# Kernel optimization log

Measured on AMD Instinct MI355X. Metric: run time of the kernel, lower is better.

The kernel has to match this reference:

```python
import jax, jax.numpy as jnp
import numpy as np

NUM_CLUSTERS = 64
DIM = 512
ALPHA = 100.0
EPS = 1e-12  # torch F.normalize eps


def setup_inputs() -> dict:
    key = jax.random.key(0)
    k1, k2 = jax.random.split(key)
    x1 = jax.random.normal(k1, (30, DIM, 28, 28), dtype=jnp.float32)
    centroids = jax.random.uniform(k2, (NUM_CLUSTERS, DIM), dtype=jnp.float32)
    # _init_params: conv weight = 2*alpha*centroids (1x1 conv), bias = -alpha*||centroid||
    conv_w = 2.0 * ALPHA * centroids
    conv_b = -ALPHA * jnp.linalg.norm(centroids, axis=1)
    return {"x1": x1, "centroids": centroids, "conv_w": conv_w, "conv_b": conv_b}


def _l2norm(v, axis):
    n = jnp.sqrt(jnp.sum(v * v, axis=axis, keepdims=True))
    return v / jnp.maximum(n, EPS)


def reference(x1, centroids, conv_w, conv_b):
    T, C, H, W = x1.shape
    K, D = centroids.shape
    x = x1.reshape(T, C, H * W)            # [T, C, N]
    x = _l2norm(x, axis=1)                 # normalize_input: L2 over channel dim
    # 1x1 conv == matmul over channels: logits [T, K, N]
    logits = jnp.einsum('kc,tcn->tkn', conv_w, x) + conv_b[None, :, None]
    a = jax.nn.softmax(logits, axis=1)     # soft assignment over clusters
    # vlad[t,k,c] = sum_n a[t,k,n]*(x[t,c,n] - centroids[k,c])
    # rewritten as two small matmuls, avoiding the [K,C,N] residual tensor
    vlad = jnp.einsum('tkn,tcn->tkc', a, x) - a.sum(axis=-1)[:, :, None] * centroids[None]
    vlad = _l2norm(vlad, axis=2)           # intra-normalization over feature dim
    v = vlad.reshape(T, K * D)
    v = _l2norm(v, axis=1)                 # global L2 normalization
    return v.sum(axis=0, keepdims=True)    # [1, K*D] accumulated over 30 timesteps
```

## Files before the change

kernel.cpp:

```cpp
#include <hip/hip_runtime.h>
#include <math.h>

#define T_ 30
#define C_ 512
#define N_ 784
#define NA_ 800
#define SPITCH 72
#define EPSV 1e-12f

typedef __attribute__((ext_vector_type(8))) short bf16x8;
typedef __attribute__((ext_vector_type(4))) float f32x4;

__device__ __forceinline__ unsigned short f2bf(float f) {
    union { float f; unsigned int u; } v; v.f = f;
    unsigned int r = (v.u + 0x7FFFu + ((v.u >> 16) & 1u)) >> 16;
    return (unsigned short)r;
}
__device__ __forceinline__ float bf2f(unsigned short h) {
    union { unsigned int u; float f; } v; v.u = ((unsigned int)h) << 16;
    return v.f;
}

__global__ void k_prep(const float* __restrict__ w, unsigned short* __restrict__ wh,
                       unsigned short* __restrict__ wl) {
    int idx = blockIdx.x * 256 + threadIdx.x;
    float v = w[idx];
    unsigned short h = f2bf(v);
    wh[idx] = h;
    wl[idx] = f2bf(v - bf2f(h));
}

__global__ __launch_bounds__(256, 4) void k_assign(
    const float* __restrict__ x, const unsigned short* __restrict__ wh,
    const unsigned short* __restrict__ wl, const float* __restrict__ b,
    unsigned short* __restrict__ aT, float* __restrict__ asum)
{
    __shared__ __align__(16) char smem[2 * 4 * 16 * SPITCH * 2];
    unsigned short* xh = (unsigned short*)smem;
    unsigned short* xl = xh + 4 * 16 * SPITCH;
    float* red = (float*)smem;
    __shared__ float ssq[4][16];

    int t = blockIdx.y, n0 = blockIdx.x * 16;
    int tid = threadIdx.x;
    int w = tid >> 6, L = tid & 63, lid = L & 15, quad = L >> 4;
    int cbase = w * 128;
    int nseg = (L & 3) * 4;
    int crow = L >> 2;

    const float* xb = x + (size_t)t * C_ * N_ + n0 + nseg;
    unsigned short* shh = xh + w * 16 * SPITCH;
    unsigned short* shl = xl + w * 16 * SPITCH;
    const unsigned short* wha = wh + (size_t)lid * C_ + cbase + quad * 8;
    const unsigned short* wla = wl + (size_t)lid * C_ + cbase + quad * 8;

    float bk = b[L];
    float ss0 = 0.f, ss1 = 0.f, ss2 = 0.f, ss3 = 0.f;
    f32x4 acc[4];
    #pragma unroll
    for (int mt = 0; mt < 4; ++mt)
        #pragma unroll
        for (int r = 0; r < 4; ++r) acc[mt][r] = 0.f;

    #pragma unroll
    for (int half = 0; half < 2; ++half) {
        float4 q[4];
        #pragma unroll
        for (int p = 0; p < 4; ++p)
            q[p] = *reinterpret_cast<const float4*>(
                xb + (size_t)(cbase + half * 64 + p * 16 + crow) * N_);
        #pragma unroll
        for (int p = 0; p < 4; ++p) {
            int cl = p * 16 + crow;
            float vv[4] = {q[p].x, q[p].y, q[p].z, q[p].w};
            ss0 = fmaf(vv[0], vv[0], ss0); ss1 = fmaf(vv[1], vv[1], ss1);
            ss2 = fmaf(vv[2], vv[2], ss2); ss3 = fmaf(vv[3], vv[3], ss3);
            #pragma unroll
            for (int j = 0; j < 4; ++j) {
                unsigned short h = f2bf(vv[j]);
                shh[(nseg + j) * SPITCH + cl] = h;
                shl[(nseg + j) * SPITCH + cl] = f2bf(vv[j] - bf2f(h));
            }
        }
        #pragma unroll
        for (int ks2 = 0; ks2 < 2; ++ks2) {
            bf16x8 bh = *reinterpret_cast<const bf16x8*>(
                &shh[lid * SPITCH + ks2 * 32 + quad * 8]);
            bf16x8 bl = *reinterpret_cast<const bf16x8*>(
                &shl[lid * SPITCH + ks2 * 32 + quad * 8]);
            int cg = half * 64 + ks2 * 32;
            #pragma unroll
            for (int mt = 0; mt < 4; ++mt) {
                bf16x8 ah = *reinterpret_cast<const bf16x8*>(
                    wha + (size_t)mt * 16 * C_ + cg);
                bf16x8 al = *reinterpret_cast<const bf16x8*>(
                    wla + (size_t)mt * 16 * C_ + cg);
                acc[mt] = __builtin_amdgcn_mfma_f32_16x16x32_bf16(ah, bh, acc[mt], 0, 0, 0);
                acc[mt] = __builtin_amdgcn_mfma_f32_16x16x32_bf16(al, bh, acc[mt], 0, 0, 0);
                acc[mt] = __builtin_amdgcn_mfma_f32_16x16x32_bf16(ah, bl, acc[mt], 0, 0, 0);
            }
        }
    }
    #pragma unroll
    for (int m = 4; m <= 32; m <<= 1) {
        ss0 += __shfl_xor(ss0, m, 64); ss1 += __shfl_xor(ss1, m, 64);
        ss2 += __shfl_xor(ss2, m, 64); ss3 += __shfl_xor(ss3, m, 64);
    }
    if (L < 4) {
        ssq[w][L * 4 + 0] = ss0; ssq[w][L * 4 + 1] = ss1;
        ssq[w][L * 4 + 2] = ss2; ssq[w][L * 4 + 3] = ss3;
    }
    __syncthreads();
    {
        float* rp = red + w * (16 * 68);
        #pragma unroll
        for (int mt = 0; mt < 4; ++mt)
            *reinterpret_cast<f32x4*>(&rp[lid * 68 + mt * 16 + quad * 4]) = acc[mt];
    }
    __syncthreads();

    float vv[4], iv[4];
    #pragma unroll
    for (int i = 0; i < 4; ++i) {
        int n = w * 4 + i;
        float s = ssq[0][n] + ssq[1][n] + ssq[2][n] + ssq[3][n];
        iv[i] = 1.0f / fmaxf(sqrtf(s), EPSV);
        float v = red[0 * 1088 + n * 68 + L] + red[1 * 1088 + n * 68 + L]
                + red[2 * 1088 + n * 68 + L] + red[3 * 1088 + n * 68 + L];
        vv[i] = fmaf(v, iv[i], bk);
    }
    float mx[4] = {vv[0], vv[1], vv[2], vv[3]};
    #pragma unroll
    for (int m = 1; m <= 32; m <<= 1) {
        #pragma unroll
        for (int i = 0; i < 4; ++i) mx[i] = fmaxf(mx[i], __shfl_xor(mx[i], m, 64));
    }
    float e[4], se[4];
    #pragma unroll
    for (int i = 0; i < 4; ++i) { e[i] = __expf(vv[i] - mx[i]); se[i] = e[i]; }
    #pragma unroll
    for (int m = 1; m <= 32; m <<= 1) {
        #pragma unroll
        for (int i = 0; i < 4; ++i) se[i] += __shfl_xor(se[i], m, 64);
    }
    float asl = 0.f;
    unsigned short av[4];
    #pragma unroll
    for (int i = 0; i < 4; ++i) {
        float a = e[i] / se[i];
        av[i] = f2bf(a * iv[i]);
        asl += a;
    }
    atomicAdd(&asum[t * 64 + L], asl);
    ushort4 st; st.x = av[0]; st.y = av[1]; st.z = av[2]; st.w = av[3];
    *reinterpret_cast<ushort4*>(aT + ((size_t)t * 64 + L) * NA_ + n0 + w * 4) = st;
    if (blockIdx.x == 48) {
        ushort4 z; z.x = 0; z.y = 0; z.z = 0; z.w = 0;
        *reinterpret_cast<ushort4*>(aT + ((size_t)t * 64 + L) * NA_ + 784 + w * 4) = z;
    }
}

__global__ __launch_bounds__(256, 4) void k_vlad(
    const float* __restrict__ x, const unsigned short* __restrict__ aT,
    const float* __restrict__ asum, const float* __restrict__ cent,
    float* __restrict__ vlad)
{
    __shared__ float red[4][16 * 68];
    int t = blockIdx.z, nh = blockIdx.y, c0 = blockIdx.x * 16;
    int tid = threadIdx.x;
    int w = tid >> 6, L = tid & 63, lid = L & 15, quad = L >> 4;

    f32x4 acc[4];
    #pragma unroll
    for (int mt = 0; mt < 4; ++mt)
        #pragma unroll
        for (int r = 0; r < 4; ++r) acc[mt][r] = 0.f;

    const float* xrow = x + ((size_t)t * C_ + c0 + lid) * N_;
    const unsigned short* a0 = aT + (size_t)t * 64 * NA_ + (size_t)lid * NA_;

    int k = tid >> 2, cs4 = (tid & 3) * 4;
    float as = nh ? 0.f : asum[t * 64 + k];
    float4 cv = *reinterpret_cast<const float4*>(cent + k * C_ + c0 + cs4);

    int send = nh ? 25 : 13;
    int s0 = nh * 13 + w;

    int nb = s0 * 32 + quad * 8;
    int nc = nb > 776 ? 776 : nb;
    float4 x0c = *reinterpret_cast<const float4*>(xrow + nc);
    float4 x1c = *reinterpret_cast<const float4*>(xrow + nc + 4);
    bf16x8 f0 = *reinterpret_cast<const bf16x8*>(a0 + nb);
    bf16x8 f1 = *reinterpret_cast<const bf16x8*>(a0 + 16 * NA_ + nb);
    bf16x8 f2 = *reinterpret_cast<const bf16x8*>(a0 + 32 * NA_ + nb);
    bf16x8 f3 = *reinterpret_cast<const bf16x8*>(a0 + 48 * NA_ + nb);

    for (int s = s0; s < send; s += 4) {
        int sn = s + 4;
        float4 x0n = x0c, x1n = x1c;
        bf16x8 g0 = f0, g1 = f1, g2v = f2, g3 = f3;
        if (sn < send) {
            int nb2 = sn * 32 + quad * 8;
            int nc2 = nb2 > 776 ? 776 : nb2;
            x0n = *reinterpret_cast<const float4*>(xrow + nc2);
            x1n = *reinterpret_cast<const float4*>(xrow + nc2 + 4);
            g0 = *reinterpret_cast<const bf16x8*>(a0 + nb2);
            g1 = *reinterpret_cast<const bf16x8*>(a0 + 16 * NA_ + nb2);
            g2v = *reinterpret_cast<const bf16x8*>(a0 + 32 * NA_ + nb2);
            g3 = *reinterpret_cast<const bf16x8*>(a0 + 48 * NA_ + nb2);
        }
        bf16x8 bb;
        bb[0] = (short)f2bf(x0c.x); bb[1] = (short)f2bf(x0c.y);
        bb[2] = (short)f2bf(x0c.z); bb[3] = (short)f2bf(x0c.w);
        bb[4] = (short)f2bf(x1c.x); bb[5] = (short)f2bf(x1c.y);
        bb[6] = (short)f2bf(x1c.z); bb[7] = (short)f2bf(x1c.w);
        acc[0] = __builtin_amdgcn_mfma_f32_16x16x32_bf16(f0, bb, acc[0], 0, 0, 0);
        acc[1] = __builtin_amdgcn_mfma_f32_16x16x32_bf16(f1, bb, acc[1], 0, 0, 0);
        acc[2] = __builtin_amdgcn_mfma_f32_16x16x32_bf16(f2, bb, acc[2], 0, 0, 0);
        acc[3] = __builtin_amdgcn_mfma_f32_16x16x32_bf16(f3, bb, acc[3], 0, 0, 0);
        x0c = x0n; x1c = x1n; f0 = g0; f1 = g1; f2 = g2v; f3 = g3;
    }
    {
        float* rp = &red[w][0];
        #pragma unroll
        for (int mt = 0; mt < 4; ++mt)
            *reinterpret_cast<f32x4*>(&rp[lid * 68 + mt * 16 + quad * 4]) = acc[mt];
    }
    __syncthreads();

    float* dst = vlad + ((size_t)t * 64 + k) * C_ + c0 + cs4;
    #pragma unroll
    for (int j = 0; j < 4; ++j) {
        int cc = cs4 + j;
        float v = red[0][cc * 68 + k] + red[1][cc * 68 + k]
                + red[2][cc * 68 + k] + red[3][cc * 68 + k];
        v -= as * ((const float*)&cv)[j];
        atomicAdd(dst + j, v);
    }
}

__global__ __launch_bounds__(256) void k_g2(const float* __restrict__ vlad,
                                            float* __restrict__ g2) {
    int tid = threadIdx.x;
    int w = tid >> 6, L = tid & 63;
    int r = blockIdx.x * 4 + w;
    const float* p = vlad + (size_t)r * C_;
    float s = 0.f;
    #pragma unroll
    for (int i = 0; i < 2; ++i) {
        float4 a = *reinterpret_cast<const float4*>(p + i * 256 + L * 4);
        s = fmaf(a.x, a.x, fmaf(a.y, a.y, fmaf(a.z, a.z, fmaf(a.w, a.w, s))));
    }
    #pragma unroll
    for (int m = 1; m <= 32; m <<= 1) s += __shfl_xor(s, m, 64);
    if (L == 0) g2[r] = s;
}

__global__ __launch_bounds__(256) void k_out(
    const float* __restrict__ vlad, const float* __restrict__ g2,
    float* __restrict__ out)
{
    __shared__ float intr[1920];
    __shared__ float gl[1920];
    __shared__ float sinv[T_];
    __shared__ float part[256];
    int tid = threadIdx.x;
    for (int i = tid; i < 1920; i += 256) {
        float s = g2[i];
        gl[i] = s;
        intr[i] = 1.0f / fmaxf(sqrtf(s), EPSV);
    }
    __syncthreads();
    if (tid < T_) {
        float s = 0.f;
        #pragma unroll 8
        for (int k = 0; k < 64; ++k) {
            float iv = intr[tid * 64 + k];
            s += gl[tid * 64 + k] * iv * iv;
        }
        sinv[tid] = 1.0f / fmaxf(sqrtf(s), EPSV);
    }
    __syncthreads();
    int idx = blockIdx.x * 128 + (tid & 127);
    int th = tid >> 7;
    int k = idx >> 9;
    float s = 0.f;
    #pragma unroll
    for (int t = th * 15; t < th * 15 + 15; ++t)
        s += vlad[(size_t)t * 32768 + idx] * intr[t * 64 + k] * sinv[t];
    part[tid] = s;
    __syncthreads();
    if (tid < 128) out[idx] = part[tid] + part[tid + 128];
}

extern "C" void kernel_launch(void* const* d_in, const int* in_sizes, int n_in,
                              void* d_out, int out_size, void* d_ws, size_t ws_size,
                              hipStream_t stream) {
    const float* x    = (const float*)d_in[0];
    const float* cent = (const float*)d_in[1];
    const float* w    = (const float*)d_in[2];
    const float* b    = (const float*)d_in[3];
    float* out = (float*)d_out;

    char* p = (char*)d_ws;
    unsigned short* wh = (unsigned short*)p;  p += 65536;
    unsigned short* wl = (unsigned short*)p;  p += 65536;
    float* asum = (float*)p;                  p += 1920 * 4;
    float* vlad = (float*)p;                  p += (size_t)T_ * 64 * C_ * 4;
    float* g2   = (float*)p;                  p += 1920 * 4;
    unsigned short* aT = (unsigned short*)p;  p += (size_t)T_ * 64 * NA_ * 2;

    k_prep<<<128, 256, 0, stream>>>(w, wh, wl);
    hipMemsetAsync(asum, 0, 1920 * 4 + (size_t)T_ * 64 * C_ * 4, stream);
    k_assign<<<dim3(49, T_), 256, 0, stream>>>(x, wh, wl, b, aT, asum);
    k_vlad<<<dim3(32, 2, T_), 256, 0, stream>>>(x, aT, asum, cent, vlad);
    k_g2<<<480, 256, 0, stream>>>(vlad, g2);
    k_out<<<256, 256, 0, stream>>>(vlad, g2, out);
}
```

Before: 158.1 us.

## Emit bf16 copy of x in assign kernel and split vlad partials without atomics

```diff
diff --git a/kernel.cpp b/kernel.cpp
--- a/kernel.cpp
+++ b/kernel.cpp
@@ -5,6 +5,7 @@
 #define C_ 512
 #define N_ 784
 #define NA_ 800
+#define XBP 800
 #define SPITCH 72
 #define EPSV 1e-12f
 
@@ -33,7 +34,8 @@
 __global__ __launch_bounds__(256, 4) void k_assign(
     const float* __restrict__ x, const unsigned short* __restrict__ wh,
     const unsigned short* __restrict__ wl, const float* __restrict__ b,
-    unsigned short* __restrict__ aT, float* __restrict__ asum)
+    unsigned short* __restrict__ aT, float* __restrict__ asum,
+    unsigned short* __restrict__ xbh)
 {
     __shared__ __align__(16) char smem[2 * 4 * 16 * SPITCH * 2];
     unsigned short* xh = (unsigned short*)smem;
@@ -49,11 +51,18 @@
     int crow = L >> 2;
 
     const float* xb = x + (size_t)t * C_ * N_ + n0 + nseg;
+    unsigned short* xbrow = xbh + (size_t)t * C_ * XBP + n0 + nseg;
     unsigned short* shh = xh + w * 16 * SPITCH;
     unsigned short* shl = xl + w * 16 * SPITCH;
     const unsigned short* wha = wh + (size_t)lid * C_ + cbase + quad * 8;
     const unsigned short* wla = wl + (size_t)lid * C_ + cbase + quad * 8;
 
+    float4 q[8];
+    #pragma unroll
+    for (int p = 0; p < 8; ++p)
+        q[p] = *reinterpret_cast<const float4*>(
+            xb + (size_t)(cbase + p * 16 + crow) * N_);
+
     float bk = b[L];
     float ss0 = 0.f, ss1 = 0.f, ss2 = 0.f, ss3 = 0.f;
     f32x4 acc[4];
@@ -64,23 +73,24 @@
 
     #pragma unroll
     for (int half = 0; half < 2; ++half) {
-        float4 q[4];
-        #pragma unroll
-        for (int p = 0; p < 4; ++p)
-            q[p] = *reinterpret_cast<const float4*>(
-                xb + (size_t)(cbase + half * 64 + p * 16 + crow) * N_);
         #pragma unroll
         for (int p = 0; p < 4; ++p) {
+            int pp = half * 4 + p;
             int cl = p * 16 + crow;
-            float vv[4] = {q[p].x, q[p].y, q[p].z, q[p].w};
+            int c  = cbase + pp * 16 + crow;
+            float vv[4] = {q[pp].x, q[pp].y, q[pp].z, q[pp].w};
             ss0 = fmaf(vv[0], vv[0], ss0); ss1 = fmaf(vv[1], vv[1], ss1);
             ss2 = fmaf(vv[2], vv[2], ss2); ss3 = fmaf(vv[3], vv[3], ss3);
+            unsigned short hs[4];
             #pragma unroll
             for (int j = 0; j < 4; ++j) {
                 unsigned short h = f2bf(vv[j]);
+                hs[j] = h;
                 shh[(nseg + j) * SPITCH + cl] = h;
                 shl[(nseg + j) * SPITCH + cl] = f2bf(vv[j] - bf2f(h));
             }
+            ushort4 hv; hv.x = hs[0]; hv.y = hs[1]; hv.z = hs[2]; hv.w = hs[3];
+            *reinterpret_cast<ushort4*>(xbrow + (size_t)c * XBP) = hv;
         }
         #pragma unroll
         for (int ks2 = 0; ks2 < 2; ++ks2) {
@@ -157,13 +167,19 @@
     if (blockIdx.x == 48) {
         ushort4 z; z.x = 0; z.y = 0; z.z = 0; z.w = 0;
         *reinterpret_cast<ushort4*>(aT + ((size_t)t * 64 + L) * NA_ + 784 + w * 4) = z;
+        #pragma unroll
+        for (int pp = 0; pp < 8; ++pp) {
+            int c = cbase + pp * 16 + crow;
+            *reinterpret_cast<ushort4*>(
+                xbh + ((size_t)t * C_ + c) * XBP + 784 + nseg) = z;
+        }
     }
 }
 
 __global__ __launch_bounds__(256, 4) void k_vlad(
-    const float* __restrict__ x, const unsigned short* __restrict__ aT,
+    const unsigned short* __restrict__ xbh, const unsigned short* __restrict__ aT,
     const float* __restrict__ asum, const float* __restrict__ cent,
-    float* __restrict__ vlad)
+    float* __restrict__ vlad0, float* __restrict__ vlad1)
 {
     __shared__ float red[4][16 * 68];
     int t = blockIdx.z, nh = blockIdx.y, c0 = blockIdx.x * 16;
@@ -176,7 +192,7 @@
         #pragma unroll
         for (int r = 0; r < 4; ++r) acc[mt][r] = 0.f;
 
-    const float* xrow = x + ((size_t)t * C_ + c0 + lid) * N_;
+    const unsigned short* xrow = xbh + ((size_t)t * C_ + c0 + lid) * XBP;
     const unsigned short* a0 = aT + (size_t)t * 64 * NA_ + (size_t)lid * NA_;
 
     int k = tid >> 2, cs4 = (tid & 3) * 4;
@@ -187,9 +203,7 @@
     int s0 = nh * 13 + w;
 
     int nb = s0 * 32 + quad * 8;
-    int nc = nb > 776 ? 776 : nb;
-    float4 x0c = *reinterpret_cast<const float4*>(xrow + nc);
-    float4 x1c = *reinterpret_cast<const float4*>(xrow + nc + 4);
+    bf16x8 xc = *reinterpret_cast<const bf16x8*>(xrow + nb);
     bf16x8 f0 = *reinterpret_cast<const bf16x8*>(a0 + nb);
     bf16x8 f1 = *reinterpret_cast<const bf16x8*>(a0 + 16 * NA_ + nb);
     bf16x8 f2 = *reinterpret_cast<const bf16x8*>(a0 + 32 * NA_ + nb);
@@ -197,28 +211,21 @@
 
     for (int s = s0; s < send; s += 4) {
         int sn = s + 4;
-        float4 x0n = x0c, x1n = x1c;
+        bf16x8 xn = xc;
         bf16x8 g0 = f0, g1 = f1, g2v = f2, g3 = f3;
         if (sn < send) {
             int nb2 = sn * 32 + quad * 8;
-            int nc2 = nb2 > 776 ? 776 : nb2;
-            x0n = *reinterpret_cast<const float4*>(xrow + nc2);
-            x1n = *reinterpret_cast<const float4*>(xrow + nc2 + 4);
-            g0 = *reinterpret_cast<const bf16x8*>(a0 + nb2);
-            g1 = *reinterpret_cast<const bf16x8*>(a0 + 16 * NA_ + nb2);
+            xn  = *reinterpret_cast<const bf16x8*>(xrow + nb2);
+            g0  = *reinterpret_cast<const bf16x8*>(a0 + nb2);
+            g1  = *reinterpret_cast<const bf16x8*>(a0 + 16 * NA_ + nb2);
             g2v = *reinterpret_cast<const bf16x8*>(a0 + 32 * NA_ + nb2);
-            g3 = *reinterpret_cast<const bf16x8*>(a0 + 48 * NA_ + nb2);
-        }
-        bf16x8 bb;
-        bb[0] = (short)f2bf(x0c.x); bb[1] = (short)f2bf(x0c.y);
-        bb[2] = (short)f2bf(x0c.z); bb[3] = (short)f2bf(x0c.w);
-        bb[4] = (short)f2bf(x1c.x); bb[5] = (short)f2bf(x1c.y);
-        bb[6] = (short)f2bf(x1c.z); bb[7] = (short)f2bf(x1c.w);
-        acc[0] = __builtin_amdgcn_mfma_f32_16x16x32_bf16(f0, bb, acc[0], 0, 0, 0);
-        acc[1] = __builtin_amdgcn_mfma_f32_16x16x32_bf16(f1, bb, acc[1], 0, 0, 0);
-        acc[2] = __builtin_amdgcn_mfma_f32_16x16x32_bf16(f2, bb, acc[2], 0, 0, 0);
-        acc[3] = __builtin_amdgcn_mfma_f32_16x16x32_bf16(f3, bb, acc[3], 0, 0, 0);
-        x0c = x0n; x1c = x1n; f0 = g0; f1 = g1; f2 = g2v; f3 = g3;
+            g3  = *reinterpret_cast<const bf16x8*>(a0 + 48 * NA_ + nb2);
+        }
+        acc[0] = __builtin_amdgcn_mfma_f32_16x16x32_bf16(f0, xc, acc[0], 0, 0, 0);
+        acc[1] = __builtin_amdgcn_mfma_f32_16x16x32_bf16(f1, xc, acc[1], 0, 0, 0);
+        acc[2] = __builtin_amdgcn_mfma_f32_16x16x32_bf16(f2, xc, acc[2], 0, 0, 0);
+        acc[3] = __builtin_amdgcn_mfma_f32_16x16x32_bf16(f3, xc, acc[3], 0, 0, 0);
+        xc = xn; f0 = g0; f1 = g1; f2 = g2v; f3 = g3;
     }
     {
         float* rp = &red[w][0];
@@ -228,28 +235,34 @@
     }
     __syncthreads();
 
-    float* dst = vlad + ((size_t)t * 64 + k) * C_ + c0 + cs4;
+    float* dst = (nh ? vlad1 : vlad0) + ((size_t)t * 64 + k) * C_ + c0 + cs4;
+    float4 vout;
     #pragma unroll
     for (int j = 0; j < 4; ++j) {
         int cc = cs4 + j;
         float v = red[0][cc * 68 + k] + red[1][cc * 68 + k]
                 + red[2][cc * 68 + k] + red[3][cc * 68 + k];
         v -= as * ((const float*)&cv)[j];
-        atomicAdd(dst + j, v);
-    }
-}
-
-__global__ __launch_bounds__(256) void k_g2(const float* __restrict__ vlad,
+        ((float*)&vout)[j] = v;
+    }
+    *reinterpret_cast<float4*>(dst) = vout;
+}
+
+__global__ __launch_bounds__(256) void k_g2(const float* __restrict__ vlad0,
+                                            const float* __restrict__ vlad1,
                                             float* __restrict__ g2) {
     int tid = threadIdx.x;
     int w = tid >> 6, L = tid & 63;
     int r = blockIdx.x * 4 + w;
-    const float* p = vlad + (size_t)r * C_;
+    const float* p0 = vlad0 + (size_t)r * C_;
+    const float* p1 = vlad1 + (size_t)r * C_;
     float s = 0.f;
     #pragma unroll
     for (int i = 0; i < 2; ++i) {
-        float4 a = *reinterpret_cast<const float4*>(p + i * 256 + L * 4);
-        s = fmaf(a.x, a.x, fmaf(a.y, a.y, fmaf(a.z, a.z, fmaf(a.w, a.w, s))));
+        float4 a = *reinterpret_cast<const float4*>(p0 + i * 256 + L * 4);
+        float4 b4 = *reinterpret_cast<const float4*>(p1 + i * 256 + L * 4);
+        float vx = a.x + b4.x, vy = a.y + b4.y, vz = a.z + b4.z, vw = a.w + b4.w;
+        s = fmaf(vx, vx, fmaf(vy, vy, fmaf(vz, vz, fmaf(vw, vw, s))));
     }
     #pragma unroll
     for (int m = 1; m <= 32; m <<= 1) s += __shfl_xor(s, m, 64);
@@ -257,8 +270,8 @@
 }
 
 __global__ __launch_bounds__(256) void k_out(
-    const float* __restrict__ vlad, const float* __restrict__ g2,
-    float* __restrict__ out)
+    const float* __restrict__ vlad0, const float* __restrict__ vlad1,
+    const float* __restrict__ g2, float* __restrict__ out)
 {
     __shared__ float intr[1920];
     __shared__ float gl[1920];
@@ -286,8 +299,10 @@
     int k = idx >> 9;
     float s = 0.f;
     #pragma unroll
-    for (int t = th * 15; t < th * 15 + 15; ++t)
-        s += vlad[(size_t)t * 32768 + idx] * intr[t * 64 + k] * sinv[t];
+    for (int t = th * 15; t < th * 15 + 15; ++t) {
+        size_t off = (size_t)t * 32768 + idx;
+        s += (vlad0[off] + vlad1[off]) * intr[t * 64 + k] * sinv[t];
+    }
     part[tid] = s;
     __syncthreads();
     if (tid < 128) out[idx] = part[tid] + part[tid + 128];
@@ -303,17 +318,19 @@
     float* out = (float*)d_out;
 
     char* p = (char*)d_ws;
-    unsigned short* wh = (unsigned short*)p;  p += 65536;
-    unsigned short* wl = (unsigned short*)p;  p += 65536;
-    float* asum = (float*)p;                  p += 1920 * 4;
-    float* vlad = (float*)p;                  p += (size_t)T_ * 64 * C_ * 4;
-    float* g2   = (float*)p;                  p += 1920 * 4;
-    unsigned short* aT = (unsigned short*)p;  p += (size_t)T_ * 64 * NA_ * 2;
+    unsigned short* wh = (unsigned short*)p;   p += 65536;
+    unsigned short* wl = (unsigned short*)p;   p += 65536;
+    float* asum  = (float*)p;                  p += 1920 * 4;
+    float* g2    = (float*)p;                  p += 1920 * 4;
+    float* vlad0 = (float*)p;                  p += (size_t)T_ * 64 * C_ * 4;
+    float* vlad1 = (float*)p;                  p += (size_t)T_ * 64 * C_ * 4;
+    unsigned short* aT = (unsigned short*)p;   p += (size_t)T_ * 64 * NA_ * 2;
+    unsigned short* xbh = (unsigned short*)p;  p += (size_t)T_ * C_ * XBP * 2;
 
     k_prep<<<128, 256, 0, stream>>>(w, wh, wl);
-    hipMemsetAsync(asum, 0, 1920 * 4 + (size_t)T_ * 64 * C_ * 4, stream);
-    k_assign<<<dim3(49, T_), 256, 0, stream>>>(x, wh, wl, b, aT, asum);
-    k_vlad<<<dim3(32, 2, T_), 256, 0, stream>>>(x, aT, asum, cent, vlad);
-    k_g2<<<480, 256, 0, stream>>>(vlad, g2);
-    k_out<<<256, 256, 0, stream>>>(vlad, g2, out);
-}
+    hipMemsetAsync(asum, 0, 1920 * 4, stream);
+    k_assign<<<dim3(49, T_), 256, 0, stream>>>(x, wh, wl, b, aT, asum, xbh);
+    k_vlad<<<dim3(32, 2, T_), 256, 0, stream>>>(xbh, aT, asum, cent, vlad0, vlad1);
+    k_g2<<<480, 256, 0, stream>>>(vlad0, vlad1, g2);
+    k_out<<<256, 256, 0, stream>>>(vlad0, vlad1, g2, out);
+}
```

Result: faster. 148.0 us (-6.3%).

## Split vlad over cluster halves, fuse squared-norm into vlad, drop memset

Applied to the files above, without the earlier changes.

```diff
diff --git a/kernel.cpp b/kernel.cpp
--- a/kernel.cpp
+++ b/kernel.cpp
@@ -54,6 +54,12 @@
     const unsigned short* wha = wh + (size_t)lid * C_ + cbase + quad * 8;
     const unsigned short* wla = wl + (size_t)lid * C_ + cbase + quad * 8;
 
+    float4 q[8];
+    #pragma unroll
+    for (int p = 0; p < 8; ++p)
+        q[p] = *reinterpret_cast<const float4*>(
+            xb + (size_t)(cbase + p * 16 + crow) * N_);
+
     float bk = b[L];
     float ss0 = 0.f, ss1 = 0.f, ss2 = 0.f, ss3 = 0.f;
     f32x4 acc[4];
@@ -64,15 +70,11 @@
 
     #pragma unroll
     for (int half = 0; half < 2; ++half) {
-        float4 q[4];
-        #pragma unroll
-        for (int p = 0; p < 4; ++p)
-            q[p] = *reinterpret_cast<const float4*>(
-                xb + (size_t)(cbase + half * 64 + p * 16 + crow) * N_);
         #pragma unroll
         for (int p = 0; p < 4; ++p) {
+            int pp = half * 4 + p;
             int cl = p * 16 + crow;
-            float vv[4] = {q[p].x, q[p].y, q[p].z, q[p].w};
+            float vv[4] = {q[pp].x, q[pp].y, q[pp].z, q[pp].w};
             ss0 = fmaf(vv[0], vv[0], ss0); ss1 = fmaf(vv[1], vv[1], ss1);
             ss2 = fmaf(vv[2], vv[2], ss2); ss3 = fmaf(vv[3], vv[3], ss3);
             #pragma unroll
@@ -163,51 +165,45 @@
 __global__ __launch_bounds__(256, 4) void k_vlad(
     const float* __restrict__ x, const unsigned short* __restrict__ aT,
     const float* __restrict__ asum, const float* __restrict__ cent,
-    float* __restrict__ vlad)
+    float* __restrict__ vlad, float* __restrict__ g2)
 {
-    __shared__ float red[4][16 * 68];
-    int t = blockIdx.z, nh = blockIdx.y, c0 = blockIdx.x * 16;
+    __shared__ float red[4][16 * 36];
+    int t = blockIdx.z, kh = blockIdx.y, c0 = blockIdx.x * 16;
     int tid = threadIdx.x;
     int w = tid >> 6, L = tid & 63, lid = L & 15, quad = L >> 4;
 
-    f32x4 acc[4];
-    #pragma unroll
-    for (int mt = 0; mt < 4; ++mt)
+    f32x4 acc[2];
+    #pragma unroll
+    for (int mt = 0; mt < 2; ++mt)
         #pragma unroll
         for (int r = 0; r < 4; ++r) acc[mt][r] = 0.f;
 
     const float* xrow = x + ((size_t)t * C_ + c0 + lid) * N_;
-    const unsigned short* a0 = aT + (size_t)t * 64 * NA_ + (size_t)lid * NA_;
-
-    int k = tid >> 2, cs4 = (tid & 3) * 4;
-    float as = nh ? 0.f : asum[t * 64 + k];
-    float4 cv = *reinterpret_cast<const float4*>(cent + k * C_ + c0 + cs4);
-
-    int send = nh ? 25 : 13;
-    int s0 = nh * 13 + w;
-
-    int nb = s0 * 32 + quad * 8;
+    const unsigned short* a0 = aT + ((size_t)t * 64 + kh * 32 + lid) * NA_;
+
+    int k_loc = tid >> 3, j8 = tid & 7, ce = j8 * 2;
+    int kg = kh * 32 + k_loc;
+    float as = asum[t * 64 + kg];
+    float2 cv = *reinterpret_cast<const float2*>(cent + kg * C_ + c0 + ce);
+
+    int nb = w * 32 + quad * 8;
     int nc = nb > 776 ? 776 : nb;
     float4 x0c = *reinterpret_cast<const float4*>(xrow + nc);
     float4 x1c = *reinterpret_cast<const float4*>(xrow + nc + 4);
     bf16x8 f0 = *reinterpret_cast<const bf16x8*>(a0 + nb);
     bf16x8 f1 = *reinterpret_cast<const bf16x8*>(a0 + 16 * NA_ + nb);
-    bf16x8 f2 = *reinterpret_cast<const bf16x8*>(a0 + 32 * NA_ + nb);
-    bf16x8 f3 = *reinterpret_cast<const bf16x8*>(a0 + 48 * NA_ + nb);
-
-    for (int s = s0; s < send; s += 4) {
+
+    for (int s = w; s < 25; s += 4) {
         int sn = s + 4;
         float4 x0n = x0c, x1n = x1c;
-        bf16x8 g0 = f0, g1 = f1, g2v = f2, g3 = f3;
-        if (sn < send) {
+        bf16x8 g0 = f0, g1 = f1;
+        if (sn < 25) {
             int nb2 = sn * 32 + quad * 8;
             int nc2 = nb2 > 776 ? 776 : nb2;
             x0n = *reinterpret_cast<const float4*>(xrow + nc2);
             x1n = *reinterpret_cast<const float4*>(xrow + nc2 + 4);
-            g0 = *reinterpret_cast<const bf16x8*>(a0 + nb2);
-            g1 = *reinterpret_cast<const bf16x8*>(a0 + 16 * NA_ + nb2);
-            g2v = *reinterpret_cast<const bf16x8*>(a0 + 32 * NA_ + nb2);
-            g3 = *reinterpret_cast<const bf16x8*>(a0 + 48 * NA_ + nb2);
+            g0  = *reinterpret_cast<const bf16x8*>(a0 + nb2);
+            g1  = *reinterpret_cast<const bf16x8*>(a0 + 16 * NA_ + nb2);
         }
         bf16x8 bb;
         bb[0] = (short)f2bf(x0c.x); bb[1] = (short)f2bf(x0c.y);
@@ -216,44 +212,32 @@
         bb[6] = (short)f2bf(x1c.z); bb[7] = (short)f2bf(x1c.w);
         acc[0] = __builtin_amdgcn_mfma_f32_16x16x32_bf16(f0, bb, acc[0], 0, 0, 0);
         acc[1] = __builtin_amdgcn_mfma_f32_16x16x32_bf16(f1, bb, acc[1], 0, 0, 0);
-        acc[2] = __builtin_amdgcn_mfma_f32_16x16x32_bf16(f2, bb, acc[2], 0, 0, 0);
-        acc[3] = __builtin_amdgcn_mfma_f32_16x16x32_bf16(f3, bb, acc[3], 0, 0, 0);
-        x0c = x0n; x1c = x1n; f0 = g0; f1 = g1; f2 = g2v; f3 = g3;
+        x0c = x0n; x1c = x1n; f0 = g0; f1 = g1;
     }
     {
         float* rp = &red[w][0];
         #pragma unroll
-        for (int mt = 0; mt < 4; ++mt)
-            *reinterpret_cast<f32x4*>(&rp[lid * 68 + mt * 16 + quad * 4]) = acc[mt];
-    }
-    __syncthreads();
-
-    float* dst = vlad + ((size_t)t * 64 + k) * C_ + c0 + cs4;
-    #pragma unroll
-    for (int j = 0; j < 4; ++j) {
-        int cc = cs4 + j;
-        float v = red[0][cc * 68 + k] + red[1][cc * 68 + k]
-                + red[2][cc * 68 + k] + red[3][cc * 68 + k];
+        for (int mt = 0; mt < 2; ++mt)
+            *reinterpret_cast<f32x4*>(&rp[lid * 36 + mt * 16 + quad * 4]) = acc[mt];
+    }
+    __syncthreads();
+
+    float2 vout;
+    float s2 = 0.f;
+    #pragma unroll
+    for (int j = 0; j < 2; ++j) {
+        int cc = ce + j;
+        float v = red[0][cc * 36 + k_loc] + red[1][cc * 36 + k_loc]
+                + red[2][cc * 36 + k_loc] + red[3][cc * 36 + k_loc];
         v -= as * ((const float*)&cv)[j];
-        atomicAdd(dst + j, v);
-    }
-}
-
-__global__ __launch_bounds__(256) void k_g2(const float* __restrict__ vlad,
-                                            float* __restrict__ g2) {
-    int tid = threadIdx.x;
-    int w = tid >> 6, L = tid & 63;
-    int r = blockIdx.x * 4 + w;
-    const float* p = vlad + (size_t)r * C_;
-    float s = 0.f;
-    #pragma unroll
-    for (int i = 0; i < 2; ++i) {
-        float4 a = *reinterpret_cast<const float4*>(p + i * 256 + L * 4);
-        s = fmaf(a.x, a.x, fmaf(a.y, a.y, fmaf(a.z, a.z, fmaf(a.w, a.w, s))));
-    }
-    #pragma unroll
-    for (int m = 1; m <= 32; m <<= 1) s += __shfl_xor(s, m, 64);
-    if (L == 0) g2[r] = s;
+        ((float*)&vout)[j] = v;
+        s2 = fmaf(v, v, s2);
+    }
+    *reinterpret_cast<float2*>(vlad + ((size_t)t * 64 + kg) * C_ + c0 + ce) = vout;
+    s2 += __shfl_xor(s2, 1, 64);
+    s2 += __shfl_xor(s2, 2, 64);
+    s2 += __shfl_xor(s2, 4, 64);
+    if (j8 == 0) atomicAdd(&g2[t * 64 + kg], s2);
 }
 
 __global__ __launch_bounds__(256) void k_out(
@@ -306,14 +290,13 @@
     unsigned short* wh = (unsigned short*)p;  p += 65536;
     unsigned short* wl = (unsigned short*)p;  p += 65536;
     float* asum = (float*)p;                  p += 1920 * 4;
+    float* g2   = (float*)p;                  p += 1920 * 4;
     float* vlad = (float*)p;                  p += (size_t)T_ * 64 * C_ * 4;
-    float* g2   = (float*)p;                  p += 1920 * 4;
     unsigned short* aT = (unsigned short*)p;  p += (size_t)T_ * 64 * NA_ * 2;
 
     k_prep<<<128, 256, 0, stream>>>(w, wh, wl);
-    hipMemsetAsync(asum, 0, 1920 * 4 + (size_t)T_ * 64 * C_ * 4, stream);
+    hipMemsetAsync(asum, 0, 2 * 1920 * 4, stream);
     k_assign<<<dim3(49, T_), 256, 0, stream>>>(x, wh, wl, b, aT, asum);
-    k_vlad<<<dim3(32, 2, T_), 256, 0, stream>>>(x, aT, asum, cent, vlad);
-    k_g2<<<480, 256, 0, stream>>>(vlad, g2);
+    k_vlad<<<dim3(32, 2, T_), 256, 0, stream>>>(x, aT, asum, cent, vlad, g2);
     k_out<<<256, 256, 0, stream>>>(vlad, g2, out);
 }
```

After: 142.1 us. -10.1%, faster.
